# Optimization experiments

Hardware: AMD Instinct MI355X
Metric: run time of the kernel (lower is better)

## Reference

```python
import jax, jax.numpy as jnp
import numpy as np

N_NODES = 100000
N_EDGES = 1600000
IN_F = 128
HID = 64
N_CLASSES = 2


def gcn_conv(x, W, b, src, dst, dinv, n):
    # x: [N, Fin]; W: [Fin, Fout]; src/dst: [E'] (with self-loops); dinv: [N]
    h = x @ W                                    # [N, Fout]
    norm = dinv[src] * dinv[dst]                 # [E'] symmetric normalization
    msg = h[src] * norm[:, None]                 # gather + scale, [E', Fout]
    out = jax.ops.segment_sum(msg, dst, num_segments=n)  # scatter-add, [N, Fout]
    return out + b


def setup_inputs() -> dict:
    key = jax.random.key(0)
    k1, k2, k3, k4 = jax.random.split(key, 4)
    x = jax.random.normal(k1, (N_NODES, IN_F), dtype=jnp.float32)
    edge_index = jax.random.randint(k2, (2, N_EDGES), 0, N_NODES, dtype=jnp.int64)
    W1 = jax.random.normal(k3, (IN_F, HID), dtype=jnp.float32) * (1.0 / np.sqrt(IN_F))
    b1 = jnp.zeros((HID,), dtype=jnp.float32)
    W2 = jax.random.normal(k4, (HID, N_CLASSES), dtype=jnp.float32) * (1.0 / np.sqrt(HID))
    b2 = jnp.zeros((N_CLASSES,), dtype=jnp.float32)
    return {"x": x, "edge_index": edge_index, "W1": W1, "b1": b1, "W2": W2, "b2": b2}


def reference(x, edge_index, W1, b1, W2, b2):
    n = x.shape[0]
    # add self-loops (PyG GCNConv default add_self_loops=True)
    loops = jnp.arange(n, dtype=edge_index.dtype)
    src = jnp.concatenate([edge_index[0], loops])
    dst = jnp.concatenate([edge_index[1], loops])
    # degrees on dst (with self-loops) -> D^{-1/2}; deg >= 1 so no div-by-zero
    deg = jax.ops.segment_sum(jnp.ones_like(dst, dtype=x.dtype), dst, num_segments=n)
    dinv = jax.lax.rsqrt(deg)
    h = gcn_conv(x, W1, b1, src, dst, dinv, n)
    h = jax.nn.relu(h)
    # dropout p=0.5 only in training mode; reference runs eval -> identity
    out = gcn_conv(h, W2, b2, src, dst, dinv, n)
    return out
```

## Files before the change

kernel.cpp:

```cpp
#include <hip/hip_runtime.h>
#include <hip/hip_fp16.h>

#define N_NODES 100000
#define N_EDGES 1600000
#define IN_F 128
#define HID 64
#define NBUCK 1563
#define NBP 1600
#define GS 512

typedef _Float16 half8 __attribute__((ext_vector_type(8)));
typedef _Float16 half4v __attribute__((ext_vector_type(4)));
typedef float f32x4 __attribute__((ext_vector_type(4)));

__global__ __launch_bounds__(256) void k_hist_g(const int* __restrict__ dst,
                                                int* __restrict__ gcnt) {
    __shared__ int h[NBP];
    for (int t = threadIdx.x; t < NBP; t += 256) h[t] = 0;
    __syncthreads();
    const int g = blockIdx.x;
    for (int e = g * 256 + threadIdx.x; e < N_EDGES; e += GS * 256)
        atomicAdd(&h[dst[e] >> 6], 1);
    __syncthreads();
    int* row = gcnt + g * NBP;
    for (int t = threadIdx.x; t < NBP; t += 256) row[t] = h[t];
}

__global__ __launch_bounds__(512) void k_gbase(const int* __restrict__ gcnt,
                                               int* __restrict__ pre,
                                               int* __restrict__ bt) {
    const int b = blockIdx.x;
    if (b >= NBUCK) { if (threadIdx.x == 0) bt[b] = 0; return; }
    __shared__ int s[512];
    const int t = threadIdx.x;
    const int g = ((t & 63) << 3) | (t >> 6);
    int v = gcnt[g * NBP + b];
    s[t] = v;
    __syncthreads();
    for (int o = 1; o < 512; o <<= 1) {
        int tt = (t >= o) ? s[t - o] : 0;
        __syncthreads();
        s[t] += tt;
        __syncthreads();
    }
    pre[g * NBP + b] = s[t] - v;
    if (t == 511) bt[b] = s[511];
}

__global__ __launch_bounds__(1024) void k_bscan(const int* __restrict__ bt,
                                                int* __restrict__ bbase,
                                                int* __restrict__ off) {
    __shared__ int s[1024];
    const int t = threadIdx.x;
    int v0 = bt[2 * t], v1 = bt[2 * t + 1];
    int p = v0 + v1;
    s[t] = p;
    __syncthreads();
    for (int o = 1; o < 1024; o <<= 1) {
        int tt = (t >= o) ? s[t - o] : 0;
        __syncthreads();
        s[t] += tt;
        __syncthreads();
    }
    int base = s[t] - p;
    bbase[2 * t] = base;
    bbase[2 * t + 1] = base + v0;
    if (t == 0) off[N_NODES] = N_EDGES;
}

__global__ __launch_bounds__(256) void k_bin(const int* __restrict__ src,
                                             const int* __restrict__ dst,
                                             const int* __restrict__ bbase,
                                             const int* __restrict__ pre,
                                             int* __restrict__ bin) {
    __shared__ int cur[NBP];
    const int g = blockIdx.x;
    const int* prow = pre + g * NBP;
    for (int t = threadIdx.x; t < NBP; t += 256)
        cur[t] = (t < NBUCK) ? (bbase[t] + prow[t]) : 0;
    __syncthreads();
    for (int e = g * 256 + threadIdx.x; e < N_EDGES; e += GS * 256) {
        int s = src[e], d = dst[e];
        int slot = atomicAdd(&cur[d >> 6], 1);
        bin[slot] = ((d & 63) << 17) | s;
    }
}

__global__ __launch_bounds__(256) void k_csr(const int* __restrict__ bin,
                                             const int* __restrict__ bbase,
                                             int* __restrict__ off,
                                             float* __restrict__ dinv,
                                             int* __restrict__ csr) {
    __shared__ int cnt64[64];
    __shared__ int cur64[64];
    const int b = blockIdx.x;
    if (threadIdx.x < 64) cnt64[threadIdx.x] = 0;
    __syncthreads();
    const int beg = bbase[b], end = bbase[b + 1];
    for (int i = beg + threadIdx.x; i < end; i += 256)
        atomicAdd(&cnt64[(bin[i] >> 17) & 63], 1);
    __syncthreads();
    if (threadIdx.x == 0) {
        int run = beg;
        #pragma unroll
        for (int j = 0; j < 64; ++j) {
            cur64[j] = run;
            run += cnt64[j];
        }
    }
    __syncthreads();
    if (threadIdx.x < 64) {
        int node = b * 64 + threadIdx.x;
        if (node < N_NODES) {
            off[node] = cur64[threadIdx.x];
            dinv[node] = rsqrtf((float)(cnt64[threadIdx.x] + 1));
        }
    }
    __syncthreads();
    for (int i = beg + threadIdx.x; i < end; i += 256) {
        int v = bin[i];
        int slot = atomicAdd(&cur64[(v >> 17) & 63], 1);
        csr[slot] = v & 0x1FFFF;
    }
}

__global__ __launch_bounds__(256) void k_gemm1(const float* __restrict__ x,
                                               const float* __restrict__ W1,
                                               const float* __restrict__ dinv,
                                               __half* __restrict__ hout) {
    __shared__ _Float16 Wl[8192];
    const int tid = threadIdx.x, wave = tid >> 6, lane = tid & 63;
    const int quad = lane >> 4, m = lane & 15;
    if (blockIdx.x == 0 && tid < 32) ((int*)hout)[(size_t)N_NODES * 32 + tid] = 0;
    for (int it = 0; it < 16; ++it) {
        int p = it * 256 + tid;
        int j2 = p & 3, ln = (p >> 2) & 63, kc = (p >> 8) & 3, nt = p >> 10;
        int k = kc * 32 + ((ln >> 4) << 3) + j2 * 2;
        int n = nt * 16 + (ln & 15);
        Wl[p * 2]     = (_Float16)W1[k * HID + n];
        Wl[p * 2 + 1] = (_Float16)W1[(k + 1) * HID + n];
    }
    __syncthreads();
    half8 bf[16];
    #pragma unroll
    for (int i = 0; i < 16; ++i) bf[i] = ((const half8*)Wl)[i * 64 + lane];

    const int ngroups = NBUCK;
    for (int g = blockIdx.x; g < ngroups; g += gridDim.x) {
        const int n0 = g * 64 + wave * 16;
        if (n0 >= N_NODES) continue;
        const float4* xrow = (const float4*)(x + (size_t)(n0 + m) * IN_F);
        f32x4 acc[4] = {{0.f,0.f,0.f,0.f},{0.f,0.f,0.f,0.f},
                        {0.f,0.f,0.f,0.f},{0.f,0.f,0.f,0.f}};
        #pragma unroll
        for (int kc = 0; kc < 4; ++kc) {
            float4 p0 = xrow[kc * 8 + quad * 2 + 0];
            float4 p1 = xrow[kc * 8 + quad * 2 + 1];
            half8 a;
            a[0] = (_Float16)p0.x; a[1] = (_Float16)p0.y;
            a[2] = (_Float16)p0.z; a[3] = (_Float16)p0.w;
            a[4] = (_Float16)p1.x; a[5] = (_Float16)p1.y;
            a[6] = (_Float16)p1.z; a[7] = (_Float16)p1.w;
            #pragma unroll
            for (int nt = 0; nt < 4; ++nt)
                acc[nt] = __builtin_amdgcn_mfma_f32_16x16x32_f16(a, bf[nt * 4 + kc], acc[nt], 0, 0, 0);
        }
        float di[4];
        #pragma unroll
        for (int r = 0; r < 4; ++r) di[r] = dinv[n0 + quad * 4 + r];
        _Float16* hp = (_Float16*)hout;
        #pragma unroll
        for (int nt = 0; nt < 4; ++nt)
            #pragma unroll
            for (int r = 0; r < 4; ++r)
                hp[(size_t)(n0 + quad * 4 + r) * HID + nt * 16 + m] =
                    (_Float16)(acc[nt][r] * di[r]);
    }
}

__global__ __launch_bounds__(256) void k_gather1(const __half* __restrict__ h1,
                                                 const int* __restrict__ off,
                                                 const int* __restrict__ csr,
                                                 const float* __restrict__ dinv,
                                                 const float* __restrict__ b1,
                                                 const float* __restrict__ W2,
                                                 float2* __restrict__ h2p) {
    const int wave = threadIdx.x >> 6, lane = threadIdx.x & 63;
    const int grp = lane >> 4, fl = lane & 15;
    const int d = blockIdx.x * 4 + wave;
    const int beg = off[d], end = off[d + 1];
    const half4v* hrows = (const half4v*)h1;
    float a0 = 0.f, a1 = 0.f, a2 = 0.f, a3 = 0.f;
    for (int base = beg; base < end; base += 64) {
        const int cnt = min(64, end - base);
        int sidx = (lane < cnt) ? csr[base + lane] : N_NODES;
        for (int j = 0; j < cnt; j += 16) {
            int ss[4];
            #pragma unroll
            for (int u = 0; u < 4; ++u)
                ss[u] = __shfl(sidx, (j + 4 * u + grp) & 63, 64);
            half4v v[4];
            #pragma unroll
            for (int u = 0; u < 4; ++u)
                v[u] = hrows[(size_t)ss[u] * 16 + fl];
            #pragma unroll
            for (int u = 0; u < 4; ++u) {
                a0 += (float)v[u][0];
                a1 += (float)v[u][1];
                a2 += (float)v[u][2];
                a3 += (float)v[u][3];
            }
        }
    }
    #pragma unroll
    for (int o = 32; o >= 16; o >>= 1) {
        a0 += __shfl_xor(a0, o, 64);
        a1 += __shfl_xor(a1, o, 64);
        a2 += __shfl_xor(a2, o, 64);
        a3 += __shfl_xor(a3, o, 64);
    }
    half4v sv = hrows[(size_t)d * 16 + fl];
    a0 += (float)sv[0]; a1 += (float)sv[1]; a2 += (float)sv[2]; a3 += (float)sv[3];
    const float di = dinv[d];
    float4 bb = ((const float4*)b1)[fl];
    float y0 = fmaxf(di * a0 + bb.x, 0.f);
    float y1 = fmaxf(di * a1 + bb.y, 0.f);
    float y2 = fmaxf(di * a2 + bb.z, 0.f);
    float y3 = fmaxf(di * a3 + bb.w, 0.f);
    float4 w01 = ((const float4*)W2)[2 * fl];
    float4 w23 = ((const float4*)W2)[2 * fl + 1];
    float c0 = y0 * w01.x + y1 * w01.z + y2 * w23.x + y3 * w23.z;
    float c1 = y0 * w01.y + y1 * w01.w + y2 * w23.y + y3 * w23.w;
    #pragma unroll
    for (int o = 8; o > 0; o >>= 1) {
        c0 += __shfl_xor(c0, o, 64);
        c1 += __shfl_xor(c1, o, 64);
    }
    if (lane == 0) h2p[d] = make_float2(c0 * di, c1 * di);
}

__global__ __launch_bounds__(256) void k_gather2(const float2* __restrict__ h2p,
                                                 const int* __restrict__ off,
                                                 const int* __restrict__ csr,
                                                 const float* __restrict__ dinv,
                                                 const float* __restrict__ b2,
                                                 float* __restrict__ out) {
    int i = blockIdx.x * 256 + threadIdx.x;
    if (i >= N_NODES) return;
    int beg = off[i], end = off[i + 1];
    float2 a = h2p[i];
    for (int s = beg; s < end; ++s) {
        float2 v = h2p[csr[s]];
        a.x += v.x;
        a.y += v.y;
    }
    float di = dinv[i];
    out[i * 2 + 0] = di * a.x + b2[0];
    out[i * 2 + 1] = di * a.y + b2[1];
}

extern "C" void kernel_launch(void* const* d_in, const int* in_sizes, int n_in,
                              void* d_out, int out_size, void* d_ws, size_t ws_size,
                              hipStream_t stream) {
    const float* x  = (const float*)d_in[0];
    const int*   ei = (const int*)d_in[1];
    const float* W1 = (const float*)d_in[2];
    const float* b1 = (const float*)d_in[3];
    const float* W2 = (const float*)d_in[4];
    const float* b2 = (const float*)d_in[5];
    float* out = (float*)d_out;

    const int* src = ei;
    const int* dst = ei + N_EDGES;

    int*    wsi   = (int*)d_ws;
    int*    gcnt  = wsi;
    int*    pre   = wsi + 819200;
    int*    bt    = wsi + 1638400;
    int*    bbase = wsi + 1640448;
    int*    off   = wsi + 1642496;
    float*  dinv  = (float*)(wsi + 1742848);
    int*    bin   = wsi + 1843200;
    int*    csr   = wsi + 3443200;
    __half* h1p   = (__half*)(wsi + 5043200);
    float2* h2p   = (float2*)(wsi + 8243264);

    dim3 B(256);
    k_hist_g <<<GS, B, 0, stream>>>(dst, gcnt);
    k_gbase  <<<2048, 512, 0, stream>>>(gcnt, pre, bt);
    k_bscan  <<<1, 1024, 0, stream>>>(bt, bbase, off);
    k_bin    <<<GS, B, 0, stream>>>(src, dst, bbase, pre, bin);
    k_csr    <<<NBUCK, B, 0, stream>>>(bin, bbase, off, dinv, csr);

    k_gemm1  <<<512, B, 0, stream>>>(x, W1, dinv, h1p);
    k_gather1<<<N_NODES / 4, B, 0, stream>>>(h1p, off, csr, dinv, b1, W2, h2p);
    k_gather2<<<(N_NODES + 255) / 256, B, 0, stream>>>(h2p, off, csr, dinv, b2, out);
}
```

Baseline: 205.9 us.

## Pack bucket counts to 16-bit, vectorize edge loads, packed-half accumulation, unroll gather2

Measured after the change: 191.2 us. 1.08x faster.

```diff
diff --git a/kernel.cpp b/kernel.cpp
--- a/kernel.cpp
+++ b/kernel.cpp
@@ -11,40 +11,57 @@
 
 typedef _Float16 half8 __attribute__((ext_vector_type(8)));
 typedef _Float16 half4v __attribute__((ext_vector_type(4)));
+typedef _Float16 half2v __attribute__((ext_vector_type(2)));
 typedef float f32x4 __attribute__((ext_vector_type(4)));
 
 __global__ __launch_bounds__(256) void k_hist_g(const int* __restrict__ dst,
-                                                int* __restrict__ gcnt) {
+                                                unsigned short* __restrict__ gcnt) {
     __shared__ int h[NBP];
     for (int t = threadIdx.x; t < NBP; t += 256) h[t] = 0;
     __syncthreads();
     const int g = blockIdx.x;
-    for (int e = g * 256 + threadIdx.x; e < N_EDGES; e += GS * 256)
-        atomicAdd(&h[dst[e] >> 6], 1);
-    __syncthreads();
-    int* row = gcnt + g * NBP;
-    for (int t = threadIdx.x; t < NBP; t += 256) row[t] = h[t];
-}
-
-__global__ __launch_bounds__(512) void k_gbase(const int* __restrict__ gcnt,
-                                               int* __restrict__ pre,
+    const int NQ = N_EDGES / 4;
+    const int4* dst4 = (const int4*)dst;
+    for (int q = g * 256 + threadIdx.x; q < NQ; q += GS * 256) {
+        int4 d4 = dst4[q];
+        atomicAdd(&h[d4.x >> 6], 1);
+        atomicAdd(&h[d4.y >> 6], 1);
+        atomicAdd(&h[d4.z >> 6], 1);
+        atomicAdd(&h[d4.w >> 6], 1);
+    }
+    __syncthreads();
+    unsigned int* row = (unsigned int*)(gcnt + g * NBP);
+    for (int t = threadIdx.x; t < NBP / 2; t += 256)
+        row[t] = (unsigned)h[2 * t] | ((unsigned)h[2 * t + 1] << 16);
+}
+
+__global__ __launch_bounds__(512) void k_gbase(const unsigned short* __restrict__ gcnt,
+                                               unsigned short* __restrict__ pre,
                                                int* __restrict__ bt) {
-    const int b = blockIdx.x;
-    if (b >= NBUCK) { if (threadIdx.x == 0) bt[b] = 0; return; }
-    __shared__ int s[512];
+    __shared__ uint4 s[512];
     const int t = threadIdx.x;
+    const int b0 = blockIdx.x * 8;
     const int g = ((t & 63) << 3) | (t >> 6);
-    int v = gcnt[g * NBP + b];
-    s[t] = v;
+    uint4 v = *(const uint4*)(gcnt + g * NBP + b0);
+    uint4 run = v;
+    s[t] = run;
     __syncthreads();
     for (int o = 1; o < 512; o <<= 1) {
-        int tt = (t >= o) ? s[t - o] : 0;
+        uint4 tt = {0u, 0u, 0u, 0u};
+        if (t >= o) tt = s[t - o];
         __syncthreads();
-        s[t] += tt;
+        run.x += tt.x; run.y += tt.y; run.z += tt.z; run.w += tt.w;
+        s[t] = run;
         __syncthreads();
     }
-    pre[g * NBP + b] = s[t] - v;
-    if (t == 511) bt[b] = s[511];
+    uint4 ex = { run.x - v.x, run.y - v.y, run.z - v.z, run.w - v.w };
+    *(uint4*)(pre + g * NBP + b0) = ex;
+    if (t == 511) {
+        bt[b0 + 0] = run.x & 0xFFFF; bt[b0 + 1] = run.x >> 16;
+        bt[b0 + 2] = run.y & 0xFFFF; bt[b0 + 3] = run.y >> 16;
+        bt[b0 + 4] = run.z & 0xFFFF; bt[b0 + 5] = run.z >> 16;
+        bt[b0 + 6] = run.w & 0xFFFF; bt[b0 + 7] = run.w >> 16;
+    }
 }
 
 __global__ __launch_bounds__(1024) void k_bscan(const int* __restrict__ bt,
@@ -52,7 +69,8 @@
                                                 int* __restrict__ off) {
     __shared__ int s[1024];
     const int t = threadIdx.x;
-    int v0 = bt[2 * t], v1 = bt[2 * t + 1];
+    int v0 = (2 * t < 1568) ? bt[2 * t] : 0;
+    int v1 = (2 * t + 1 < 1568) ? bt[2 * t + 1] : 0;
     int p = v0 + v1;
     s[t] = p;
     __syncthreads();
@@ -71,18 +89,25 @@
 __global__ __launch_bounds__(256) void k_bin(const int* __restrict__ src,
                                              const int* __restrict__ dst,
                                              const int* __restrict__ bbase,
-                                             const int* __restrict__ pre,
+                                             const unsigned short* __restrict__ pre,
                                              int* __restrict__ bin) {
     __shared__ int cur[NBP];
     const int g = blockIdx.x;
-    const int* prow = pre + g * NBP;
+    const unsigned short* prow = pre + g * NBP;
     for (int t = threadIdx.x; t < NBP; t += 256)
-        cur[t] = (t < NBUCK) ? (bbase[t] + prow[t]) : 0;
-    __syncthreads();
-    for (int e = g * 256 + threadIdx.x; e < N_EDGES; e += GS * 256) {
-        int s = src[e], d = dst[e];
-        int slot = atomicAdd(&cur[d >> 6], 1);
-        bin[slot] = ((d & 63) << 17) | s;
+        cur[t] = (t < NBUCK) ? (bbase[t] + (int)prow[t]) : 0;
+    __syncthreads();
+    const int NQ = N_EDGES / 4;
+    const int4* src4 = (const int4*)src;
+    const int4* dst4 = (const int4*)dst;
+    for (int q = g * 256 + threadIdx.x; q < NQ; q += GS * 256) {
+        int4 s4 = src4[q];
+        int4 d4 = dst4[q];
+        int slot;
+        slot = atomicAdd(&cur[d4.x >> 6], 1); bin[slot] = ((d4.x & 63) << 17) | s4.x;
+        slot = atomicAdd(&cur[d4.y >> 6], 1); bin[slot] = ((d4.y & 63) << 17) | s4.y;
+        slot = atomicAdd(&cur[d4.z >> 6], 1); bin[slot] = ((d4.z & 63) << 17) | s4.z;
+        slot = atomicAdd(&cur[d4.w >> 6], 1); bin[slot] = ((d4.w & 63) << 17) | s4.w;
     }
 }
 
@@ -188,6 +213,11 @@
     const int wave = threadIdx.x >> 6, lane = threadIdx.x & 63;
     const int grp = lane >> 4, fl = lane & 15;
     const int d = blockIdx.x * 4 + wave;
+    if (d > N_NODES) return;
+    if (d == N_NODES) {
+        if (lane == 0) h2p[d] = make_float2(0.f, 0.f);
+        return;
+    }
     const int beg = off[d], end = off[d + 1];
     const half4v* hrows = (const half4v*)h1;
     float a0 = 0.f, a1 = 0.f, a2 = 0.f, a3 = 0.f;
@@ -203,13 +233,15 @@
             #pragma unroll
             for (int u = 0; u < 4; ++u)
                 v[u] = hrows[(size_t)ss[u] * 16 + fl];
+            half2v p0 = {(_Float16)0.f, (_Float16)0.f};
+            half2v p1 = {(_Float16)0.f, (_Float16)0.f};
             #pragma unroll
             for (int u = 0; u < 4; ++u) {
-                a0 += (float)v[u][0];
-                a1 += (float)v[u][1];
-                a2 += (float)v[u][2];
-                a3 += (float)v[u][3];
+                p0 += __builtin_shufflevector(v[u], v[u], 0, 1);
+                p1 += __builtin_shufflevector(v[u], v[u], 2, 3);
             }
+            a0 += (float)p0[0]; a1 += (float)p0[1];
+            a2 += (float)p1[0]; a3 += (float)p1[1];
         }
     }
     #pragma unroll
@@ -249,14 +281,23 @@
     if (i >= N_NODES) return;
     int beg = off[i], end = off[i + 1];
     float2 a = h2p[i];
-    for (int s = beg; s < end; ++s) {
-        float2 v = h2p[csr[s]];
-        a.x += v.x;
-        a.y += v.y;
+    for (int s = beg; s < end; s += 4) {
+        int node[4];
+        #pragma unroll
+        for (int u = 0; u < 4; ++u) {
+            int idx = s + u;
+            int n = csr[min(idx, end - 1)];
+            node[u] = (idx < end) ? n : N_NODES;
+        }
+        float2 v[4];
+        #pragma unroll
+        for (int u = 0; u < 4; ++u) v[u] = h2p[node[u]];
+        #pragma unroll
+        for (int u = 0; u < 4; ++u) { a.x += v[u].x; a.y += v[u].y; }
     }
     float di = dinv[i];
-    out[i * 2 + 0] = di * a.x + b2[0];
-    out[i * 2 + 1] = di * a.y + b2[1];
+    float2 o2 = make_float2(di * a.x + b2[0], di * a.y + b2[1]);
+    ((float2*)out)[i] = o2;
 }
 
 extern "C" void kernel_launch(void* const* d_in, const int* in_sizes, int n_in,
@@ -273,26 +314,26 @@
     const int* src = ei;
     const int* dst = ei + N_EDGES;
 
-    int*    wsi   = (int*)d_ws;
-    int*    gcnt  = wsi;
-    int*    pre   = wsi + 819200;
-    int*    bt    = wsi + 1638400;
-    int*    bbase = wsi + 1640448;
-    int*    off   = wsi + 1642496;
-    float*  dinv  = (float*)(wsi + 1742848);
-    int*    bin   = wsi + 1843200;
-    int*    csr   = wsi + 3443200;
-    __half* h1p   = (__half*)(wsi + 5043200);
-    float2* h2p   = (float2*)(wsi + 8243264);
+    int*            wsi   = (int*)d_ws;
+    unsigned short* gcnt  = (unsigned short*)wsi;
+    unsigned short* pre   = (unsigned short*)(wsi + 409600);
+    int*            bt    = wsi + 819200;
+    int*            bbase = wsi + 821248;
+    int*            off   = wsi + 823296;
+    float*          dinv  = (float*)(wsi + 923648);
+    int*            bin   = wsi + 1024000;
+    int*            csr   = wsi + 2624000;
+    __half*         h1p   = (__half*)(wsi + 4224000);
+    float2*         h2p   = (float2*)(wsi + 7424064);
 
     dim3 B(256);
     k_hist_g <<<GS, B, 0, stream>>>(dst, gcnt);
-    k_gbase  <<<2048, 512, 0, stream>>>(gcnt, pre, bt);
+    k_gbase  <<<196, 512, 0, stream>>>(gcnt, pre, bt);
     k_bscan  <<<1, 1024, 0, stream>>>(bt, bbase, off);
     k_bin    <<<GS, B, 0, stream>>>(src, dst, bbase, pre, bin);
     k_csr    <<<NBUCK, B, 0, stream>>>(bin, bbase, off, dinv, csr);
 
     k_gemm1  <<<512, B, 0, stream>>>(x, W1, dinv, h1p);
-    k_gather1<<<N_NODES / 4, B, 0, stream>>>(h1p, off, csr, dinv, b1, W2, h2p);
+    k_gather1<<<N_NODES / 4 + 1, B, 0, stream>>>(h1p, off, csr, dinv, b1, W2, h2p);
     k_gather2<<<(N_NODES + 255) / 256, B, 0, stream>>>(h2p, off, csr, dinv, b2, out);
 }
```
